# Kernel optimization log

Measured on AMD Instinct MI355X. Metric: run time of the kernel, lower is better.

Reference implementation:

```python
import jax, jax.numpy as jnp
import numpy as np

EPS = 1e-6
NHEADS = 16


def setup_inputs() -> dict:
    key = jax.random.key(0)
    ks = jax.random.split(key, 6)
    b, n, dim, h = 2, 2048, 2048, NHEADS
    d = dim // h
    x = jax.random.normal(ks[0], (b, n, dim), dtype=jnp.float32)
    qkv_w = jax.random.normal(ks[1], (3 * dim, dim), dtype=jnp.float32) * (dim ** -0.5)
    qkv_b = jax.random.normal(ks[2], (3 * dim,), dtype=jnp.float32) * 0.01
    q_norm_w = jnp.ones((d,), dtype=jnp.float32)
    k_norm_w = jnp.ones((d,), dtype=jnp.float32)
    # Flux-style rotation matrices: (1, 1, n, d/2, 2, 2)
    pos = jnp.arange(n, dtype=jnp.float32)[:, None]
    inv_freq = 1.0 / (10000.0 ** (jnp.arange(0, d, 2, dtype=jnp.float32) / d))  # [d/2]
    ang = pos * inv_freq[None, :]  # [n, d/2]
    cos, sin = jnp.cos(ang), jnp.sin(ang)
    rot = jnp.stack([jnp.stack([cos, -sin], axis=-1),
                     jnp.stack([sin, cos], axis=-1)], axis=-1)  # [n, d/2, 2, 2]
    rot = rot[None, None]  # [1,1,n,d/2,2,2]
    return {"x": x, "qkv_w": qkv_w, "qkv_b": qkv_b,
            "q_norm_w": q_norm_w, "k_norm_w": k_norm_w, "rot": rot}


def _rmsnorm(t, w):
    t32 = t.astype(jnp.float32)
    inv = jax.lax.rsqrt(jnp.mean(t32 * t32, axis=-1, keepdims=True) + EPS)
    return ((t32 * inv) * w).astype(t.dtype)


def _apply_rope(t, rot):
    # t: [b,h,n,d]; rot: [1,1,n,d/2,2,2]
    b, h, n, d = t.shape
    tx = t.astype(jnp.float32).reshape(b, h, n, d // 2, 1, 2)
    out = rot[..., 0] * tx[..., 0] + rot[..., 1] * tx[..., 1]  # [b,h,n,d/2,2]
    return out.reshape(b, h, n, d).astype(t.dtype)


def reference(x, qkv_w, qkv_b, q_norm_w, k_norm_w, rot):
    b, n, dim = x.shape
    d = q_norm_w.shape[0]
    h = dim // d
    qkv = x @ qkv_w.T + qkv_b  # [b, n, 3*dim]
    # layout per Rearrange 'b n (h d j) -> b h n d j'
    qkv = qkv.reshape(b, n, h, d, 3).transpose(0, 2, 1, 3, 4)  # [b,h,n,d,3]
    q, k, v = qkv[..., 0], qkv[..., 1], qkv[..., 2]
    q = _apply_rope(_rmsnorm(q, q_norm_w), rot)
    k = _apply_rope(_rmsnorm(k, k_norm_w), rot)
    scores = jnp.einsum('bhqd,bhkd->bhqk', q, k) * (d ** -0.5)
    attn = jax.nn.softmax(scores, axis=-1)
    out = jnp.einsum('bhqk,bhkd->bhqd', attn, v)
    return out.transpose(0, 2, 1, 3).reshape(b, n, dim)  # b n (h d)
```

## Files before the change

kernel.cpp:

```cpp
#include <hip/hip_runtime.h>
#include <cstdint>
#include <cstddef>


#define LOG2E 1.4426950408889634f
#define ATT_SCALE 0.08838834764831845f
#define QSCALE (ATT_SCALE * LOG2E)

typedef __attribute__((ext_vector_type(8))) __bf16 bf16x8;
typedef __attribute__((ext_vector_type(4))) __bf16 bf16x4;
typedef __attribute__((ext_vector_type(4))) float f32x4;

__device__ __forceinline__ float b2f(unsigned u) {
  u <<= 16;
  return __builtin_bit_cast(float, u);
}
__device__ __forceinline__ unsigned short f2b(float f) {
  unsigned x = __builtin_bit_cast(unsigned, f);
  return (unsigned short)((x + 0x7fffu + ((x >> 16) & 1u)) >> 16);
}
__device__ __forceinline__ void gl16(const void* g, void* l) {
  __builtin_amdgcn_global_load_lds((__attribute__((address_space(1))) void*)(g),
                                   (__attribute__((address_space(3))) void*)(l), 16, 0, 0);
}

__global__ void k_cvt(const float4* __restrict__ in, ushort4* __restrict__ out, int n4) {
  int i = blockIdx.x * blockDim.x + threadIdx.x;
  int st = gridDim.x * blockDim.x;
  for (; i < n4; i += st) {
    float4 v = in[i];
    ushort4 o;
    o.x = f2b(v.x); o.y = f2b(v.y); o.z = f2b(v.z); o.w = f2b(v.w);
    out[i] = o;
  }
}

__global__ __launch_bounds__(512, 2) void k_gemm(const unsigned short* __restrict__ A,
                                                 const unsigned short* __restrict__ W,
                                                 const float* __restrict__ bias,
                                                 unsigned short* __restrict__ C) {
  __shared__ __align__(16) unsigned short lds[65536];
  const int tid = threadIdx.x;
  const int w = tid >> 6, l = tid & 63;
  const int lo = l & 15, hi = l >> 4;
  const int WM = w >> 2, WN = w & 3;
  const int wg = blockIdx.x;
  const int swz = (wg & 7) * 48 + (wg >> 3);
  const int mbase = (swz / 24) * 256, nbase = (swz % 24) * 256;

  const int srow = w * 16 + (l >> 2);
  const int scol = ((l & 3) * 8) ^ ((srow & 3) << 3);

  auto stage = [&](int t) {
    unsigned short* Sa = lds + (t & 3) * 16384;
    unsigned short* Sb = Sa + 8192;
    const int kt = t * 32;
#pragma unroll
    for (int rd = 0; rd < 2; ++rd) {
      gl16(A + (size_t)(mbase + rd * 128 + srow) * 2048 + kt + scol,
           Sa + (rd * 128 + w * 16) * 32);
      gl16(W + (size_t)(nbase + rd * 128 + srow) * 2048 + kt + scol,
           Sb + (rd * 128 + w * 16) * 32);
    }
  };

  f32x4 acc[8][4] = {};
  stage(0); stage(1); stage(2);

  const int ea = (hi * 8) ^ ((lo & 3) << 3);
  for (int t = 0; t < 64; ++t) {
    if (t < 62)       asm volatile("s_waitcnt vmcnt(8) lgkmcnt(0)" ::: "memory");
    else if (t == 62) asm volatile("s_waitcnt vmcnt(4) lgkmcnt(0)" ::: "memory");
    else              asm volatile("s_waitcnt vmcnt(0) lgkmcnt(0)" ::: "memory");
    __builtin_amdgcn_s_barrier();
    asm volatile("" ::: "memory");
    if (t + 3 < 64) stage(t + 3);
    asm volatile("" ::: "memory");

    const unsigned short* Sa = lds + (t & 3) * 16384;
    const unsigned short* Sb = Sa + 8192;
    bf16x8 af[8], bf[4];
#pragma unroll
    for (int i = 0; i < 8; ++i)
      af[i] = *(const bf16x8*)&Sa[(WM * 128 + i * 16 + lo) * 32 + ea];
#pragma unroll
    for (int j = 0; j < 4; ++j)
      bf[j] = *(const bf16x8*)&Sb[(WN * 64 + j * 16 + lo) * 32 + ea];
    __builtin_amdgcn_s_setprio(1);
#pragma unroll
    for (int i = 0; i < 8; ++i)
#pragma unroll
      for (int j = 0; j < 4; ++j)
        acc[i][j] = __builtin_amdgcn_mfma_f32_16x16x32_bf16(af[i], bf[j], acc[i][j], 0, 0, 0);
    __builtin_amdgcn_s_setprio(0);
  }

  const int rowb = mbase + WM * 128;
  const int colb = nbase + WN * 64;
#pragma unroll
  for (int j = 0; j < 4; ++j) {
    float bj = bias[colb + j * 16 + lo];
#pragma unroll
    for (int i = 0; i < 8; ++i)
#pragma unroll
      for (int r = 0; r < 4; ++r) {
        int row = rowb + i * 16 + hi * 4 + r;
        C[(size_t)row * 6144 + colb + j * 16 + lo] = f2b(acc[i][j][r] + bj);
      }
  }
}

__global__ __launch_bounds__(64) void k_normrope(const unsigned short* __restrict__ qkv,
                                                 const float* __restrict__ qw,
                                                 const float* __restrict__ kw,
                                                 const float* __restrict__ rot,
                                                 unsigned short* __restrict__ Q,
                                                 unsigned short* __restrict__ K,
                                                 unsigned short* __restrict__ V) {
  const int l = threadIdx.x;
  const int h = blockIdx.x & 15;
  const int n = (blockIdx.x >> 4) & 2047;
  const int b = blockIdx.x >> 15;
  const unsigned* p = (const unsigned*)(qkv + (size_t)(b * 2048 + n) * 6144 + h * 384 + l * 6);
  unsigned u0 = p[0], u1 = p[1], u2 = p[2];
  float q0 = b2f(u0 & 0xffff), k0 = b2f(u0 >> 16);
  float v0 = b2f(u1 & 0xffff), q1 = b2f(u1 >> 16);
  float k1 = b2f(u2 & 0xffff), v1 = b2f(u2 >> 16);
  (void)v0; (void)v1;
  float sq = q0 * q0 + q1 * q1, sk = k0 * k0 + k1 * k1;
#pragma unroll
  for (int m = 1; m < 64; m <<= 1) {
    sq += __shfl_xor(sq, m, 64);
    sk += __shfl_xor(sk, m, 64);
  }
  float qi = rsqrtf(sq * (1.0f / 128.0f) + 1e-6f) * QSCALE;
  float ki = rsqrtf(sk * (1.0f / 128.0f) + 1e-6f);
  float2 qwv = *(const float2*)&qw[2 * l];
  float2 kwv = *(const float2*)&kw[2 * l];
  float4 r = *(const float4*)&rot[n * 256 + l * 4];
  float qn0 = q0 * qi * qwv.x, qn1 = q1 * qi * qwv.y;
  float kn0 = k0 * ki * kwv.x, kn1 = k1 * ki * kwv.y;
  unsigned qo = (unsigned)f2b(r.x * qn0 + r.y * qn1) | ((unsigned)f2b(r.z * qn0 + r.w * qn1) << 16);
  unsigned ko = (unsigned)f2b(r.x * kn0 + r.y * kn1) | ((unsigned)f2b(r.z * kn0 + r.w * kn1) << 16);
  unsigned vo = (u1 & 0xffffu) | (u2 & 0xffff0000u);
  size_t ob = ((size_t)(b * 16 + h) * 2048 + n) * 128 + 2 * l;
  *(unsigned*)(Q + ob) = qo;
  *(unsigned*)(K + ob) = ko;
  *(unsigned*)(V + ob) = vo;
}

__global__ __launch_bounds__(256) void k_transpose(const unsigned short* __restrict__ V,
                                                   unsigned short* __restrict__ Vt) {
  __shared__ unsigned short tile[64 * 66];
  const int t = threadIdx.x;
  const int d0 = blockIdx.x * 64;
  const int n0 = blockIdx.y * 64;
  const int bh = blockIdx.z;
#pragma unroll
  for (int s = t; s < 512; s += 256) {
    int nr = s >> 3, c8 = (s & 7) * 8;
    uint4 vv = *(const uint4*)(V + ((size_t)bh * 2048 + n0 + nr) * 128 + d0 + c8);
    unsigned* tp = (unsigned*)&tile[nr * 66 + c8];
    tp[0] = vv.x; tp[1] = vv.y; tp[2] = vv.z; tp[3] = vv.w;
  }
  __syncthreads();
#pragma unroll
  for (int s = t; s < 512; s += 256) {
    int dr = s >> 3, n8 = (s & 7) * 8;
    unsigned short e[8];
#pragma unroll
    for (int j = 0; j < 8; ++j) e[j] = tile[(n8 + j) * 66 + dr];
    uint4 o;
    o.x = e[0] | ((unsigned)e[1] << 16);
    o.y = e[2] | ((unsigned)e[3] << 16);
    o.z = e[4] | ((unsigned)e[5] << 16);
    o.w = e[6] | ((unsigned)e[7] << 16);
    *(uint4*)(Vt + ((size_t)bh * 128 + d0 + dr) * 2048 + n0 + n8) = o;
  }
}

__global__ __launch_bounds__(512, 4) void k_attn(const unsigned short* __restrict__ Q,
                                                 const unsigned short* __restrict__ K,
                                                 const unsigned short* __restrict__ Vt,
                                                 float* __restrict__ out) {
  __shared__ __align__(16) unsigned short lds[40960];
  unsigned short* Ps = lds + 32768;
  const int tid = threadIdx.x;
  const int w = tid >> 6, l = tid & 63;
  const int lo = l & 15, hi = l >> 4;
  const int swz = (lo & 7) << 3;
  const int qt = blockIdx.x, bh = blockIdx.y;
  const unsigned short* Qb = Q + (size_t)bh * 2048 * 128;
  const unsigned short* Kb = K + (size_t)bh * 2048 * 128;
  const unsigned short* Vb = Vt + (size_t)bh * 128 * 2048;
  unsigned short* Psw = Ps + w * 1024;

  bf16x8 qf[4];
  const int qrow = qt * 128 + w * 16 + lo;
#pragma unroll
  for (int dk = 0; dk < 4; ++dk)
    qf[dk] = *(const bf16x8*)&Qb[(size_t)qrow * 128 + dk * 32 + hi * 8];

  f32x4 Oacc[8] = {};
  float m_run = -__builtin_inff(), l_run = 0.0f;

  const int krow0 = w * 4 + hi;
  const int vrow0 = w * 8 + (l >> 3);
  const unsigned short* kp = Kb + (size_t)krow0 * 128 + ((lo * 8) ^ ((krow0 & 7) << 3));
  const unsigned short* vp = Vb + (size_t)vrow0 * 2048 + (((l & 7) * 8) ^ ((vrow0 & 7) << 3));

  auto stage = [&](int t, int b) {
    unsigned short* Ksb = lds + b * 16384;
    unsigned short* Vtsb = Ksb + 8192;
#pragma unroll
    for (int r = 0; r < 2; ++r) {
      gl16(kp + (size_t)t * 8192 + r * 4096,
           Ksb + (r * 32 + w * 4) * 128);
      gl16(vp + (size_t)r * 131072 + t * 64,
           Vtsb + (r * 64 + w * 8) * 64);
    }
  };

  stage(0, 0);
  int cur = 0;
  for (int t = 0; t < 32; ++t) {
    __syncthreads();
    if (t + 1 < 32) stage(t + 1, cur ^ 1);
    const unsigned short* Ks = lds + cur * 16384;
    const unsigned short* Vts = Ks + 8192;

    f32x4 S[4] = {};
#pragma unroll
    for (int kf = 0; kf < 4; ++kf)
#pragma unroll
      for (int dk = 0; dk < 4; ++dk)
        S[kf] = __builtin_amdgcn_mfma_f32_16x16x32_bf16(
            *(const bf16x8*)&Ks[(kf * 16 + lo) * 128 + ((dk * 32 + hi * 8) ^ swz)],
            qf[dk], S[kf], 0, 0, 0);

    float m01, m23, mt;
    m01 = fmaxf(fmaxf(S[0][0], S[0][1]), fmaxf(S[0][2], S[0][3]));
    m23 = fmaxf(fmaxf(S[1][0], S[1][1]), fmaxf(S[1][2], S[1][3]));
    mt = fmaxf(m01, m23);
    m01 = fmaxf(fmaxf(S[2][0], S[2][1]), fmaxf(S[2][2], S[2][3]));
    m23 = fmaxf(fmaxf(S[3][0], S[3][1]), fmaxf(S[3][2], S[3][3]));
    mt = fmaxf(mt, fmaxf(m01, m23));
    mt = fmaxf(mt, __shfl_xor(mt, 16, 64));
    mt = fmaxf(mt, __shfl_xor(mt, 32, 64));

    const bool defer = __all(mt <= m_run + 8.0f);
    float m_new = m_run, alpha = 1.0f;
    if (!defer) {
      m_new = fmaxf(m_run, mt);
      alpha = exp2f(m_run - m_new);
    }

    float p[4][4];
    float ls = 0.0f;
#pragma unroll
    for (int kf = 0; kf < 4; ++kf)
#pragma unroll
      for (int r = 0; r < 4; ++r) {
        p[kf][r] = exp2f(S[kf][r] - m_new);
        ls += p[kf][r];
      }
    ls += __shfl_xor(ls, 16, 64);
    ls += __shfl_xor(ls, 32, 64);

#pragma unroll
    for (int kf = 0; kf < 4; ++kf) {
      bf16x4 pk;
      pk[0] = (__bf16)p[kf][0]; pk[1] = (__bf16)p[kf][1];
      pk[2] = (__bf16)p[kf][2]; pk[3] = (__bf16)p[kf][3];
      *(bf16x4*)&Psw[lo * 64 + ((kf * 16 + hi * 4) ^ swz)] = pk;
    }

    if (!defer) {
#pragma unroll
      for (int df = 0; df < 8; ++df) {
        Oacc[df][0] *= alpha; Oacc[df][1] *= alpha;
        Oacc[df][2] *= alpha; Oacc[df][3] *= alpha;
      }
      l_run = l_run * alpha + ls;
      m_run = m_new;
    } else {
      l_run += ls;
    }

    const bf16x8 pb0 = *(const bf16x8*)&Psw[lo * 64 + ((hi * 8) ^ swz)];
    const bf16x8 pb1 = *(const bf16x8*)&Psw[lo * 64 + ((32 + hi * 8) ^ swz)];
#pragma unroll
    for (int df = 0; df < 8; ++df) {
      Oacc[df] = __builtin_amdgcn_mfma_f32_16x16x32_bf16(
          *(const bf16x8*)&Vts[(df * 16 + lo) * 64 + ((hi * 8) ^ swz)], pb0, Oacc[df], 0, 0, 0);
      Oacc[df] = __builtin_amdgcn_mfma_f32_16x16x32_bf16(
          *(const bf16x8*)&Vts[(df * 16 + lo) * 64 + ((32 + hi * 8) ^ swz)], pb1, Oacc[df], 0, 0, 0);
    }
    cur ^= 1;
  }

  const float inv = 1.0f / l_run;
  __syncthreads();
  float* Ot = ((float*)lds) + w * 2048;
#pragma unroll
  for (int df = 0; df < 8; ++df)
#pragma unroll
    for (int r = 0; r < 4; ++r)
      Ot[lo * 128 + df * 16 + hi * 4 + r] = Oacc[df][r] * inv;
  const int b = bh >> 4, h = bh & 15;
  const int q2 = l >> 2, c = (l & 3) * 32;
  float* op = out + ((size_t)(b * 2048 + qt * 128 + w * 16 + q2) * 2048 + h * 128 + c);
#pragma unroll
  for (int u = 0; u < 8; ++u)
    *(float4*)&op[u * 4] = *(const float4*)&Ot[q2 * 128 + c + u * 4];
}

extern "C" void kernel_launch(void* const* d_in, const int* in_sizes, int n_in,
                              void* d_out, int out_size, void* d_ws, size_t ws_size,
                              hipStream_t stream) {
  (void)in_sizes; (void)n_in; (void)out_size; (void)ws_size;
  const float* x = (const float*)d_in[0];
  const float* qkv_w = (const float*)d_in[1];
  const float* qkv_b = (const float*)d_in[2];
  const float* q_norm_w = (const float*)d_in[3];
  const float* k_norm_w = (const float*)d_in[4];
  const float* rot = (const float*)d_in[5];
  float* out = (float*)d_out;
  char* ws = (char*)d_ws;
  unsigned short* xb  = (unsigned short*)(ws);
  unsigned short* wb  = (unsigned short*)(ws + 16777216);
  unsigned short* qkv = (unsigned short*)(ws + 41943040);
  unsigned short* Qb  = (unsigned short*)(ws + 92274688);
  unsigned short* Kb  = (unsigned short*)(ws + 109051904);
  unsigned short* Vb  = (unsigned short*)(ws + 125829120);
  unsigned short* Vtb = (unsigned short*)(ws);

  hipLaunchKernelGGL(k_cvt, dim3(1024), dim3(256), 0, stream,
                     (const float4*)x, (ushort4*)xb, 8388608 / 4);
  hipLaunchKernelGGL(k_cvt, dim3(1024), dim3(256), 0, stream,
                     (const float4*)qkv_w, (ushort4*)wb, 12582912 / 4);
  hipLaunchKernelGGL(k_gemm, dim3(384), dim3(512), 0, stream, xb, wb, qkv_b, qkv);
  hipLaunchKernelGGL(k_normrope, dim3(65536), dim3(64), 0, stream,
                     qkv, q_norm_w, k_norm_w, rot, Qb, Kb, Vb);
  hipLaunchKernelGGL(k_transpose, dim3(2, 32, 32), dim3(256), 0, stream, Vb, Vtb);
  hipLaunchKernelGGL(k_attn, dim3(16, 32), dim3(512), 0, stream, Qb, Kb, Vtb, out);
}
```

Before: 282.9 us.

## Split GEMM k-step into two half-phases interleaving loads with MFMAs; batch normrope blocks

The GEMM main loop now splits each k-step into two halves. Each half issues part of the LDS fragment reads and half of the next-stage global-to-LDS prefetch, then runs its share of MFMAs. Extra barriers and sched_barriers pin the ordering so memory traffic overlaps compute more evenly. Separately, the norm/rope kernel packs four 64-thread rows into each 256-thread block to cut block count and launch overhead. The added barriers could cost synchronization time, and the vmcnt wait counts still assume the old per-stage load grouping.

```diff
diff --git a/kernel.cpp b/kernel.cpp
--- a/kernel.cpp
+++ b/kernel.cpp
@@ -51,48 +51,68 @@
   const int srow = w * 16 + (l >> 2);
   const int scol = ((l & 3) * 8) ^ ((srow & 3) << 3);
 
-  auto stage = [&](int t) {
+  auto stage_half = [&](int t, int rd) {
     unsigned short* Sa = lds + (t & 3) * 16384;
     unsigned short* Sb = Sa + 8192;
     const int kt = t * 32;
-#pragma unroll
-    for (int rd = 0; rd < 2; ++rd) {
-      gl16(A + (size_t)(mbase + rd * 128 + srow) * 2048 + kt + scol,
-           Sa + (rd * 128 + w * 16) * 32);
-      gl16(W + (size_t)(nbase + rd * 128 + srow) * 2048 + kt + scol,
-           Sb + (rd * 128 + w * 16) * 32);
-    }
+    gl16(A + (size_t)(mbase + rd * 128 + srow) * 2048 + kt + scol,
+         Sa + (rd * 128 + w * 16) * 32);
+    gl16(W + (size_t)(nbase + rd * 128 + srow) * 2048 + kt + scol,
+         Sb + (rd * 128 + w * 16) * 32);
   };
 
   f32x4 acc[8][4] = {};
-  stage(0); stage(1); stage(2);
+  stage_half(0, 0); stage_half(0, 1);
+  stage_half(1, 0); stage_half(1, 1);
+  stage_half(2, 0); stage_half(2, 1);
 
   const int ea = (hi * 8) ^ ((lo & 3) << 3);
   for (int t = 0; t < 64; ++t) {
     if (t < 62)       asm volatile("s_waitcnt vmcnt(8) lgkmcnt(0)" ::: "memory");
     else if (t == 62) asm volatile("s_waitcnt vmcnt(4) lgkmcnt(0)" ::: "memory");
     else              asm volatile("s_waitcnt vmcnt(0) lgkmcnt(0)" ::: "memory");
+    __builtin_amdgcn_sched_barrier(0);
     __builtin_amdgcn_s_barrier();
-    asm volatile("" ::: "memory");
-    if (t + 3 < 64) stage(t + 3);
-    asm volatile("" ::: "memory");
+    __builtin_amdgcn_sched_barrier(0);
 
     const unsigned short* Sa = lds + (t & 3) * 16384;
     const unsigned short* Sb = Sa + 8192;
     bf16x8 af[8], bf[4];
-#pragma unroll
-    for (int i = 0; i < 8; ++i)
+
+#pragma unroll
+    for (int i = 0; i < 4; ++i)
       af[i] = *(const bf16x8*)&Sa[(WM * 128 + i * 16 + lo) * 32 + ea];
 #pragma unroll
     for (int j = 0; j < 4; ++j)
       bf[j] = *(const bf16x8*)&Sb[(WN * 64 + j * 16 + lo) * 32 + ea];
+    if (t + 3 < 64) stage_half(t + 3, 0);
+    __builtin_amdgcn_sched_barrier(0);
+    __builtin_amdgcn_s_barrier();
+    __builtin_amdgcn_sched_barrier(0);
     __builtin_amdgcn_s_setprio(1);
 #pragma unroll
-    for (int i = 0; i < 8; ++i)
+    for (int i = 0; i < 4; ++i)
 #pragma unroll
       for (int j = 0; j < 4; ++j)
         acc[i][j] = __builtin_amdgcn_mfma_f32_16x16x32_bf16(af[i], bf[j], acc[i][j], 0, 0, 0);
     __builtin_amdgcn_s_setprio(0);
+    __builtin_amdgcn_sched_barrier(0);
+
+#pragma unroll
+    for (int i = 4; i < 8; ++i)
+      af[i] = *(const bf16x8*)&Sa[(WM * 128 + i * 16 + lo) * 32 + ea];
+    if (t + 3 < 64) stage_half(t + 3, 1);
+    __builtin_amdgcn_sched_barrier(0);
+    __builtin_amdgcn_s_barrier();
+    __builtin_amdgcn_sched_barrier(0);
+    __builtin_amdgcn_s_setprio(1);
+#pragma unroll
+    for (int i = 4; i < 8; ++i)
+#pragma unroll
+      for (int j = 0; j < 4; ++j)
+        acc[i][j] = __builtin_amdgcn_mfma_f32_16x16x32_bf16(af[i], bf[j], acc[i][j], 0, 0, 0);
+    __builtin_amdgcn_s_setprio(0);
+    __builtin_amdgcn_sched_barrier(0);
   }
 
   const int rowb = mbase + WM * 128;
@@ -110,17 +130,18 @@
   }
 }
 
-__global__ __launch_bounds__(64) void k_normrope(const unsigned short* __restrict__ qkv,
-                                                 const float* __restrict__ qw,
-                                                 const float* __restrict__ kw,
-                                                 const float* __restrict__ rot,
-                                                 unsigned short* __restrict__ Q,
-                                                 unsigned short* __restrict__ K,
-                                                 unsigned short* __restrict__ V) {
-  const int l = threadIdx.x;
-  const int h = blockIdx.x & 15;
-  const int n = (blockIdx.x >> 4) & 2047;
-  const int b = blockIdx.x >> 15;
+__global__ __launch_bounds__(256) void k_normrope(const unsigned short* __restrict__ qkv,
+                                                  const float* __restrict__ qw,
+                                                  const float* __restrict__ kw,
+                                                  const float* __restrict__ rot,
+                                                  unsigned short* __restrict__ Q,
+                                                  unsigned short* __restrict__ K,
+                                                  unsigned short* __restrict__ V) {
+  const int l = threadIdx.x & 63;
+  const int idx = blockIdx.x * 4 + (threadIdx.x >> 6);
+  const int h = idx & 15;
+  const int n = (idx >> 4) & 2047;
+  const int b = idx >> 15;
   const unsigned* p = (const unsigned*)(qkv + (size_t)(b * 2048 + n) * 6144 + h * 384 + l * 6);
   unsigned u0 = p[0], u1 = p[1], u2 = p[2];
   float q0 = b2f(u0 & 0xffff), k0 = b2f(u0 >> 16);
@@ -340,7 +361,7 @@
   hipLaunchKernelGGL(k_cvt, dim3(1024), dim3(256), 0, stream,
                      (const float4*)qkv_w, (ushort4*)wb, 12582912 / 4);
   hipLaunchKernelGGL(k_gemm, dim3(384), dim3(512), 0, stream, xb, wb, qkv_b, qkv);
-  hipLaunchKernelGGL(k_normrope, dim3(65536), dim3(64), 0, stream,
+  hipLaunchKernelGGL(k_normrope, dim3(16384), dim3(256), 0, stream,
                      qkv, q_norm_w, k_norm_w, rot, Qb, Kb, Vb);
   hipLaunchKernelGGL(k_transpose, dim3(2, 32, 32), dim3(256), 0, stream, Vb, Vtb);
   hipLaunchKernelGGL(k_attn, dim3(16, 32), dim3(512), 0, stream, Qb, Kb, Vtb, out);
```

New measurement: 278.9 us. About the same (-1.4%).
